# Kernel optimization log

Hardware: AMD Instinct MI355X
Metric: run time of the kernel (lower is better)

## Reference

```python
import jax, jax.numpy as jnp
import numpy as np

N = 50000
E = 400000
IN_DIM = 64
HID = 64
HEADS = 4
LN_EPS = 1e-5


def _glorot(key, shape):
    fan_in, fan_out = shape[-1], shape[0] if len(shape) > 1 else shape[-1]
    lim = jnp.sqrt(6.0 / (fan_in + fan_out))
    return jax.random.uniform(key, shape, jnp.float32, -lim, lim)


def setup_inputs() -> dict:
    key = jax.random.key(0)
    ks = jax.random.split(key, 24)
    x = jax.random.normal(ks[0], (N, IN_DIM), jnp.float32)
    edge_index = jax.random.randint(ks[1], (2, E), 0, N, jnp.int64)
    role_ids = jax.random.randint(ks[2], (N,), 0, 2, jnp.int64)
    # GAT layer 1: in IN_DIM -> HEADS*HID, concat
    W1 = _glorot(ks[3], (HEADS * HID, IN_DIM))
    a1s = _glorot(ks[4], (HEADS, HID))
    a1d = _glorot(ks[5], (HEADS, HID))
    b1 = jnp.zeros((HEADS * HID,), jnp.float32)
    # GAT layer 2: HEADS*HID -> HEADS*HID, concat
    W2 = _glorot(ks[6], (HEADS * HID, HEADS * HID))
    a2s = _glorot(ks[7], (HEADS, HID))
    a2d = _glorot(ks[8], (HEADS, HID))
    b2 = jnp.zeros((HEADS * HID,), jnp.float32)
    # GAT layer 3: HEADS*HID -> HID, 1 head, no concat
    W3 = _glorot(ks[9], (HID, HEADS * HID))
    a3s = _glorot(ks[10], (1, HID))
    a3d = _glorot(ks[11], (1, HID))
    b3 = jnp.zeros((HID,), jnp.float32)
    ln1_w = jnp.ones((HEADS * HID,), jnp.float32); ln1_b = jnp.zeros((HEADS * HID,), jnp.float32)
    ln2_w = jnp.ones((HEADS * HID,), jnp.float32); ln2_b = jnp.zeros((HEADS * HID,), jnp.float32)
    ln3_w = jnp.ones((HID,), jnp.float32); ln3_b = jnp.zeros((HID,), jnp.float32)
    role_table = jax.random.normal(ks[12], (2, HID), jnp.float32)
    p1_w = _glorot(ks[13], (HID, 2 * HID)); p1_b = jnp.zeros((HID,), jnp.float32)
    p2_w = _glorot(ks[14], (HID, HID)); p2_b = jnp.zeros((HID,), jnp.float32)
    return dict(x=x, edge_index=edge_index, role_ids=role_ids,
                W1=W1, a1s=a1s, a1d=a1d, b1=b1,
                W2=W2, a2s=a2s, a2d=a2d, b2=b2,
                W3=W3, a3s=a3s, a3d=a3d, b3=b3,
                ln1_w=ln1_w, ln1_b=ln1_b, ln2_w=ln2_w, ln2_b=ln2_b,
                ln3_w=ln3_w, ln3_b=ln3_b,
                role_table=role_table, p1_w=p1_w, p1_b=p1_b, p2_w=p2_w, p2_b=p2_b)


def gat_conv(x, src, dst, W, a_src, a_dst, bias, heads, out_ch, concat):
    # x: [N, F_in]; src/dst: [E'] (self loops already appended)
    n = x.shape[0]
    h = (x @ W.T).reshape(n, heads, out_ch)              # [N,H,C]
    score_s = jnp.einsum('nhc,hc->nh', h, a_src)          # [N,H]
    score_d = jnp.einsum('nhc,hc->nh', h, a_dst)
    e = jax.nn.leaky_relu(score_s[src] + score_d[dst], 0.2)   # [E,H]
    m = jax.ops.segment_max(e, dst, num_segments=n)       # per-dst softmax
    e = jnp.exp(e - m[dst])
    s = jax.ops.segment_sum(e, dst, num_segments=n)
    alpha = e / (s[dst] + 1e-16)                          # [E,H]
    msg = h[src] * alpha[:, :, None]                      # [E,H,C]
    out = jax.ops.segment_sum(msg, dst, num_segments=n)   # [N,H,C]
    out = out.reshape(n, heads * out_ch) if concat else out.mean(axis=1)
    return out + bias


def layer_norm(x, w, b):
    mu = jnp.mean(x, axis=-1, keepdims=True)
    var = jnp.mean(jnp.square(x - mu), axis=-1, keepdims=True)
    return (x - mu) * jax.lax.rsqrt(var + LN_EPS) * w + b


def reference(x, edge_index, role_ids, W1, a1s, a1d, b1, W2, a2s, a2d, b2,
              W3, a3s, a3d, b3, ln1_w, ln1_b, ln2_w, ln2_b, ln3_w, ln3_b,
              role_table, p1_w, p1_b, p2_w, p2_b):
    n = x.shape[0]
    loop = jnp.arange(n, dtype=edge_index.dtype)
    src = jnp.concatenate([edge_index[0], loop])
    dst = jnp.concatenate([edge_index[1], loop])
    h = jax.nn.elu(gat_conv(x, src, dst, W1, a1s, a1d, b1, HEADS, HID, True))
    h = layer_norm(h, ln1_w, ln1_b)
    h = jax.nn.elu(gat_conv(h, src, dst, W2, a2s, a2d, b2, HEADS, HID, True))
    h = layer_norm(h, ln2_w, ln2_b)
    h = gat_conv(h, src, dst, W3, a3s, a3d, b3, 1, HID, False)
    h = layer_norm(h, ln3_w, ln3_b)
    role_emb = role_table[role_ids]                        # [N,HID]
    z = jnp.concatenate([h, role_emb], axis=-1)            # [N,2*HID]
    z = jax.nn.relu(z @ p1_w.T + p1_b)
    z = z @ p2_w.T + p2_b
    return z
```

## Files before the change

kernel.cpp:

```cpp
#include <hip/hip_runtime.h>
#include <math.h>


using short8 = __attribute__((ext_vector_type(8))) short;
using f32x4  = __attribute__((ext_vector_type(4))) float;

__device__ __forceinline__ unsigned short f2bf(float f) {
    unsigned int u = __builtin_bit_cast(unsigned int, f);
    u += 0x7fffu + ((u >> 16) & 1u);
    return (unsigned short)(u >> 16);
}
__device__ __forceinline__ float bf2f(unsigned int b16) {
    unsigned int u = b16 << 16;
    return __builtin_bit_cast(float, u);
}

__global__ void k_f2bf(const float* __restrict__ in, unsigned short* __restrict__ out,
                       int n) {
    int i = (blockIdx.x * 256 + threadIdx.x) * 4;
    if (i >= n) return;
    float4 v = *reinterpret_cast<const float4*>(in + i);
    ushort4 u;
    u.x = f2bf(v.x); u.y = f2bf(v.y); u.z = f2bf(v.z); u.w = f2bf(v.w);
    *reinterpret_cast<ushort4*>(out + i) = u;
}

__global__ void k_f2bf_w(const float* __restrict__ s0, unsigned short* __restrict__ d0, int n0,
                         const float* __restrict__ s1, unsigned short* __restrict__ d1, int n1,
                         const float* __restrict__ s2, unsigned short* __restrict__ d2, int n2,
                         const float* __restrict__ s3, unsigned short* __restrict__ d3, int n3,
                         const float* __restrict__ s4, unsigned short* __restrict__ d4, int n4) {
    int i = (blockIdx.x * 256 + threadIdx.x) * 4;
    const float* s; unsigned short* d; int off = i;
    if (off < n0) { s = s0; d = d0; }
    else if ((off -= n0) < n1) { s = s1; d = d1; }
    else if ((off -= n1) < n2) { s = s2; d = d2; }
    else if ((off -= n2) < n3) { s = s3; d = d3; }
    else if ((off -= n3) < n4) { s = s4; d = d4; }
    else return;
    float4 v = *reinterpret_cast<const float4*>(s + off);
    ushort4 u;
    u.x = f2bf(v.x); u.y = f2bf(v.y); u.z = f2bf(v.z); u.w = f2bf(v.w);
    *reinterpret_cast<ushort4*>(d + off) = u;
}

__global__ void k_count(const int* __restrict__ ei, int* __restrict__ deg,
                        int N, int E, int E2) {
    int i = blockIdx.x * 256 + threadIdx.x;
    if (i >= E2) return;
    int d = (i < E) ? ei[E + i] : (i - E);
    atomicAdd(&deg[d], 1);
}

__device__ __forceinline__ int blk_scan_incl(int v, int tid) {
    int lane = tid & 63, w = tid >> 6;
#pragma unroll
    for (int off = 1; off < 64; off <<= 1) {
        int u = __shfl_up(v, off);
        if (lane >= off) v += u;
    }
    __shared__ int wsum[4];
    if (lane == 63) wsum[w] = v;
    __syncthreads();
    int add = 0;
#pragma unroll
    for (int k = 0; k < 4; ++k)
        if (k < w) add += wsum[k];
    return v + add;
}

__global__ __launch_bounds__(256) void k_bsum(const int* __restrict__ deg,
                                              int* __restrict__ bsum, int N) {
    int i = blockIdx.x * 256 + threadIdx.x;
    int v = (i < N) ? deg[i] : 0;
#pragma unroll
    for (int off = 32; off; off >>= 1) v += __shfl_down(v, off);
    __shared__ int ws[4];
    if ((threadIdx.x & 63) == 0) ws[threadIdx.x >> 6] = v;
    __syncthreads();
    if (threadIdx.x == 0) bsum[blockIdx.x] = ws[0] + ws[1] + ws[2] + ws[3];
}

__global__ __launch_bounds__(256) void k_bscan(const int* __restrict__ bsum,
                                               int* __restrict__ boff, int nb) {
    int t = threadIdx.x;
    int v = (t < nb) ? bsum[t] : 0;
    int incl = blk_scan_incl(v, t);
    if (t < nb) boff[t] = incl - v;
}

__global__ __launch_bounds__(256) void k_scatter(const int* __restrict__ deg,
                                                 const int* __restrict__ boff,
                                                 int* __restrict__ row_ptr,
                                                 int* __restrict__ cursor,
                                                 int N, int E2) {
    int tid = threadIdx.x;
    int i = blockIdx.x * 256 + tid;
    int d = (i < N) ? deg[i] : 0;
    int incl = blk_scan_incl(d, tid);
    int ex = incl - d + boff[blockIdx.x];
    if (i < N) { row_ptr[i] = ex; cursor[i] = ex; }
    if (i == 0) row_ptr[N] = E2;
}

__global__ void k_fill(const int* __restrict__ ei, int* __restrict__ cursor,
                       int* __restrict__ edge_src, int N, int E, int E2) {
    int i = blockIdx.x * 256 + threadIdx.x;
    if (i >= E2) return;
    int s_, d_;
    if (i < E) { s_ = ei[i]; d_ = ei[E + i]; }
    else       { s_ = d_ = i - E; }
    int pos = atomicAdd(&cursor[d_], 1);
    edge_src[pos] = s_;
}

template <int K, bool RELU, bool BF16OUT>
__global__ __launch_bounds__(256) void k_gmfma(const unsigned short* __restrict__ A,
                                               const unsigned short* __restrict__ Wb,
                                               const float* __restrict__ bias,
                                               void* __restrict__ Cv,
                                               int M, int NC) {
    constexpr int NSTEP = K / 32;
    __shared__ unsigned short As[2][64 * 32];
    __shared__ unsigned short Bs[2][64 * 32];
    int tid = threadIdx.x;
    int lane = tid & 63, wid = tid >> 6;
    int wm = wid & 1, wn = wid >> 1;
    int fr = lane & 15, fq = lane >> 4;
    int bm = blockIdx.x * 64, bn = blockIdx.y * 64;

    int lrow = lane >> 2, lkq = (lane & 3) * 8;

    auto stage = [&](int buf, int k0) {
        int ra = wid * 16;
        int arow = min(bm + ra + lrow, M - 1);
        __builtin_amdgcn_global_load_lds(
            (const __attribute__((address_space(1))) unsigned int*)
                (A + (size_t)arow * K + k0 + lkq),
            (__attribute__((address_space(3))) unsigned int*)&As[buf][ra * 32],
            16, 0, 0);
        __builtin_amdgcn_global_load_lds(
            (const __attribute__((address_space(1))) unsigned int*)
                (Wb + (size_t)(bn + ra + lrow) * K + k0 + lkq),
            (__attribute__((address_space(3))) unsigned int*)&Bs[buf][ra * 32],
            16, 0, 0);
    };

    f32x4 acc[2][2];
#pragma unroll
    for (int mt = 0; mt < 2; ++mt)
#pragma unroll
        for (int nt = 0; nt < 2; ++nt) acc[mt][nt] = f32x4{0.f, 0.f, 0.f, 0.f};

    stage(0, 0);
    __syncthreads();
    int cur = 0;
    for (int t = 0; t < NSTEP; ++t) {
        if (t + 1 < NSTEP) stage(cur ^ 1, (t + 1) * 32);
        short8 af[2], bfr[2];
#pragma unroll
        for (int mt = 0; mt < 2; ++mt)
            af[mt] = *reinterpret_cast<const short8*>(
                &As[cur][(wm * 32 + mt * 16 + fr) * 32 + fq * 8]);
#pragma unroll
        for (int nt = 0; nt < 2; ++nt)
            bfr[nt] = *reinterpret_cast<const short8*>(
                &Bs[cur][(wn * 32 + nt * 16 + fr) * 32 + fq * 8]);
#pragma unroll
        for (int mt = 0; mt < 2; ++mt)
#pragma unroll
            for (int nt = 0; nt < 2; ++nt)
                acc[mt][nt] = __builtin_amdgcn_mfma_f32_16x16x32_bf16(
                    af[mt], bfr[nt], acc[mt][nt], 0, 0, 0);
        __syncthreads();
        cur ^= 1;
    }

#pragma unroll
    for (int nt = 0; nt < 2; ++nt) {
        int col = bn + wn * 32 + nt * 16 + fr;
        float bv = bias ? bias[col] : 0.f;
#pragma unroll
        for (int mt = 0; mt < 2; ++mt) {
#pragma unroll
            for (int j = 0; j < 4; ++j) {
                int row = bm + wm * 32 + mt * 16 + fq * 4 + j;
                if (row < M) {
                    float v = acc[mt][nt][j] + bv;
                    if (RELU) v = fmaxf(v, 0.f);
                    if constexpr (BF16OUT)
                        ((unsigned short*)Cv)[(size_t)row * NC + col] = f2bf(v);
                    else
                        ((float*)Cv)[(size_t)row * NC + col] = v;
                }
            }
        }
    }
}

__global__ __launch_bounds__(256) void k_scores4(const unsigned short* __restrict__ h,
                                                 const float* __restrict__ a_s,
                                                 const float* __restrict__ a_d,
                                                 float* __restrict__ sS,
                                                 float* __restrict__ sD, int N) {
    int wid = threadIdx.x >> 6, lane = threadIdx.x & 63;
    int n = blockIdx.x * 4 + wid;
    if (n >= N) return;
    int hh = lane >> 4;
    int cw = (lane & 15) * 4;
    uint2 u = *reinterpret_cast<const uint2*>(h + (size_t)n * 256 + lane * 4);
    float4 as4 = *reinterpret_cast<const float4*>(a_s + hh * 64 + cw);
    float4 ad4 = *reinterpret_cast<const float4*>(a_d + hh * 64 + cw);
    float h0 = bf2f(u.x & 0xffffu), h1 = bf2f(u.x >> 16);
    float h2 = bf2f(u.y & 0xffffu), h3 = bf2f(u.y >> 16);
    float ds = h0 * as4.x + h1 * as4.y + h2 * as4.z + h3 * as4.w;
    float dd = h0 * ad4.x + h1 * ad4.y + h2 * ad4.z + h3 * ad4.w;
#pragma unroll
    for (int off = 1; off < 16; off <<= 1) {
        ds += __shfl_xor(ds, off);
        dd += __shfl_xor(dd, off);
    }
    if ((lane & 15) == 0) { sS[n * 4 + hh] = ds; sD[n * 4 + hh] = dd; }
}

__global__ __launch_bounds__(256) void k_scores1(const unsigned short* __restrict__ h,
                                                 const float* __restrict__ a_s,
                                                 const float* __restrict__ a_d,
                                                 float* __restrict__ sS,
                                                 float* __restrict__ sD, int N) {
    int wid = threadIdx.x >> 6, lane = threadIdx.x & 63;
    int n = blockIdx.x * 16 + wid * 4 + (lane >> 4);
    if (n >= N) return;
    int cw = (lane & 15) * 4;
    uint2 u = *reinterpret_cast<const uint2*>(h + (size_t)n * 64 + cw);
    float4 as4 = *reinterpret_cast<const float4*>(a_s + cw);
    float4 ad4 = *reinterpret_cast<const float4*>(a_d + cw);
    float h0 = bf2f(u.x & 0xffffu), h1 = bf2f(u.x >> 16);
    float h2 = bf2f(u.y & 0xffffu), h3 = bf2f(u.y >> 16);
    float ds = h0 * as4.x + h1 * as4.y + h2 * as4.z + h3 * as4.w;
    float dd = h0 * ad4.x + h1 * ad4.y + h2 * ad4.z + h3 * ad4.w;
#pragma unroll
    for (int off = 1; off < 16; off <<= 1) {
        ds += __shfl_xor(ds, off);
        dd += __shfl_xor(dd, off);
    }
    if ((lane & 15) == 0) { sS[n] = ds; sD[n] = dd; }
}

template <int D, bool ELU, bool ROLE>
__global__ __launch_bounds__(256) void k_agg2(
        const unsigned short* __restrict__ hbf,
        const float* __restrict__ sS, const float* __restrict__ sD,
        const float* __restrict__ bias,
        const float* __restrict__ ln_w, const float* __restrict__ ln_b,
        const int* __restrict__ row_ptr, const int* __restrict__ edge_src,
        const int* __restrict__ role_ids, const float* __restrict__ role_table,
        unsigned short* __restrict__ out, int N, int ostride) {
    constexpr int H = D / 64;
    constexpr int CPT = 8;
    constexpr int TPN = D / CPT;
    constexpr int NPB = 256 / TPN;
    int tid = threadIdx.x;
    int n = blockIdx.x * NPB + tid / TPN;
    int t = tid % TPN;
    if (n >= N) return;
    int rs = row_ptr[n], re = row_ptr[n + 1];

    float sd[H];
    if constexpr (H == 4) {
        float4 s4 = *reinterpret_cast<const float4*>(sD + (size_t)n * 4);
        sd[0] = s4.x; sd[1] = s4.y; sd[2] = s4.z; sd[3] = s4.w;
    } else {
        sd[0] = sD[n];
    }

    float m[H], s[H];
#pragma unroll
    for (int h = 0; h < H; ++h) { m[h] = -1e30f; s[h] = 0.f; }
    for (int i = rs + t; i < re; i += TPN) {
        int src = edge_src[i];
        float ev[H];
        if constexpr (H == 4) {
            float4 s4 = *reinterpret_cast<const float4*>(sS + (size_t)src * 4);
            ev[0] = s4.x; ev[1] = s4.y; ev[2] = s4.z; ev[3] = s4.w;
        } else {
            ev[0] = sS[src];
        }
#pragma unroll
        for (int h = 0; h < H; ++h) {
            float e = ev[h] + sd[h];
            e = e > 0.f ? e : 0.2f * e;
            float mn = fmaxf(m[h], e);
            s[h] = s[h] * __expf(m[h] - mn) + __expf(e - mn);
            m[h] = mn;
        }
    }
#pragma unroll
    for (int off = 1; off < TPN; off <<= 1) {
#pragma unroll
        for (int h = 0; h < H; ++h) {
            float mo = __shfl_xor(m[h], off);
            float so = __shfl_xor(s[h], off);
            float mn = fmaxf(m[h], mo);
            s[h] = s[h] * __expf(m[h] - mn) + so * __expf(mo - mn);
            m[h] = mn;
        }
    }

    int c0 = CPT * t;
    int hh = c0 >> 6;
    float mh = m[hh];
    float inv = 1.f / (s[hh] + 1e-16f);
    float sdn = sd[hh];
    float a[CPT] = {};
#pragma unroll 2
    for (int i = rs; i < re; ++i) {
        int src = edge_src[i];
        float e = sS[(size_t)src * H + hh] + sdn;
        e = e > 0.f ? e : 0.2f * e;
        float p = __expf(e - mh);
        uint4 u = *reinterpret_cast<const uint4*>(hbf + (size_t)src * D + c0);
        a[0] += p * bf2f(u.x & 0xffffu); a[1] += p * bf2f(u.x >> 16);
        a[2] += p * bf2f(u.y & 0xffffu); a[3] += p * bf2f(u.y >> 16);
        a[4] += p * bf2f(u.z & 0xffffu); a[5] += p * bf2f(u.z >> 16);
        a[6] += p * bf2f(u.w & 0xffffu); a[7] += p * bf2f(u.w >> 16);
    }
    float v[CPT];
    float sum = 0.f, sq = 0.f;
#pragma unroll
    for (int j = 0; j < CPT; ++j) {
        float w = a[j] * inv + bias[c0 + j];
        if (ELU) w = w > 0.f ? w : (__expf(w) - 1.f);
        v[j] = w;
        sum += w; sq += w * w;
    }
#pragma unroll
    for (int off = 1; off < TPN; off <<= 1) {
        sum += __shfl_xor(sum, off);
        sq += __shfl_xor(sq, off);
    }
    float mu = sum / D;
    float var = fmaxf(sq / D - mu * mu, 0.f);
    float rstd = rsqrtf(var + 1e-5f);
    unsigned int w01, w23, w45, w67;
    {
        float y0 = (v[0] - mu) * rstd * ln_w[c0 + 0] + ln_b[c0 + 0];
        float y1 = (v[1] - mu) * rstd * ln_w[c0 + 1] + ln_b[c0 + 1];
        w01 = (unsigned int)f2bf(y0) | ((unsigned int)f2bf(y1) << 16);
        float y2 = (v[2] - mu) * rstd * ln_w[c0 + 2] + ln_b[c0 + 2];
        float y3 = (v[3] - mu) * rstd * ln_w[c0 + 3] + ln_b[c0 + 3];
        w23 = (unsigned int)f2bf(y2) | ((unsigned int)f2bf(y3) << 16);
        float y4 = (v[4] - mu) * rstd * ln_w[c0 + 4] + ln_b[c0 + 4];
        float y5 = (v[5] - mu) * rstd * ln_w[c0 + 5] + ln_b[c0 + 5];
        w45 = (unsigned int)f2bf(y4) | ((unsigned int)f2bf(y5) << 16);
        float y6 = (v[6] - mu) * rstd * ln_w[c0 + 6] + ln_b[c0 + 6];
        float y7 = (v[7] - mu) * rstd * ln_w[c0 + 7] + ln_b[c0 + 7];
        w67 = (unsigned int)f2bf(y6) | ((unsigned int)f2bf(y7) << 16);
    }
    uint4 o;
    o.x = w01; o.y = w23; o.z = w45; o.w = w67;
    *reinterpret_cast<uint4*>(out + (size_t)n * ostride + c0) = o;

    if constexpr (ROLE) {
        int rid = role_ids[n];
        float4 r0 = *reinterpret_cast<const float4*>(role_table + rid * 64 + c0);
        float4 r1 = *reinterpret_cast<const float4*>(role_table + rid * 64 + c0 + 4);
        uint4 ro;
        ro.x = (unsigned int)f2bf(r0.x) | ((unsigned int)f2bf(r0.y) << 16);
        ro.y = (unsigned int)f2bf(r0.z) | ((unsigned int)f2bf(r0.w) << 16);
        ro.z = (unsigned int)f2bf(r1.x) | ((unsigned int)f2bf(r1.y) << 16);
        ro.w = (unsigned int)f2bf(r1.z) | ((unsigned int)f2bf(r1.w) << 16);
        *reinterpret_cast<uint4*>(out + (size_t)n * ostride + 64 + c0) = ro;
    }
}

extern "C" void kernel_launch(void* const* d_in, const int* in_sizes, int n_in,
                              void* d_out, int out_size, void* d_ws, size_t ws_size,
                              hipStream_t stream) {
    const float* x        = (const float*)d_in[0];
    const int*   ei       = (const int*)d_in[1];
    const int*   role_ids = (const int*)d_in[2];
    const float* W1  = (const float*)d_in[3];
    const float* a1s = (const float*)d_in[4];
    const float* a1d = (const float*)d_in[5];
    const float* b1  = (const float*)d_in[6];
    const float* W2  = (const float*)d_in[7];
    const float* a2s = (const float*)d_in[8];
    const float* a2d = (const float*)d_in[9];
    const float* b2  = (const float*)d_in[10];
    const float* W3  = (const float*)d_in[11];
    const float* a3s = (const float*)d_in[12];
    const float* a3d = (const float*)d_in[13];
    const float* b3  = (const float*)d_in[14];
    const float* ln1w = (const float*)d_in[15];
    const float* ln1b = (const float*)d_in[16];
    const float* ln2w = (const float*)d_in[17];
    const float* ln2b = (const float*)d_in[18];
    const float* ln3w = (const float*)d_in[19];
    const float* ln3b = (const float*)d_in[20];
    const float* role_table = (const float*)d_in[21];
    const float* p1w = (const float*)d_in[22];
    const float* p1b = (const float*)d_in[23];
    const float* p2w = (const float*)d_in[24];
    const float* p2b = (const float*)d_in[25];

    const int N = in_sizes[0] / 64;
    const int E = in_sizes[1] / 2;
    const int E2 = E + N;

    char* p = (char*)d_ws;
    auto carve = [&](size_t bytes) -> char* {
        char* r = p;
        p += (bytes + 255) & ~(size_t)255;
        return r;
    };
    int* deg      = (int*)carve((size_t)N * 4);
    int* row_ptr  = (int*)carve((size_t)(N + 1) * 4);
    int* cursor   = (int*)carve((size_t)N * 4);
    int* edge_src = (int*)carve((size_t)E2 * 4);
    int* bsum     = (int*)carve((size_t)1024 * 4);
    int* boff     = (int*)carve((size_t)1024 * 4);
    float* sS     = (float*)carve((size_t)N * 4 * 4);
    float* sD     = (float*)carve((size_t)N * 4 * 4);
    unsigned short* hbf  = (unsigned short*)carve((size_t)N * 256 * 2);
    unsigned short* hlnb = (unsigned short*)carve((size_t)N * 256 * 2);
    unsigned short* catb = (unsigned short*)carve((size_t)N * 128 * 2);
    unsigned short* xb   = (unsigned short*)carve((size_t)N * 64 * 2);
    unsigned short* W1b  = (unsigned short*)carve((size_t)256 * 64 * 2);
    unsigned short* W2b  = (unsigned short*)carve((size_t)256 * 256 * 2);
    unsigned short* W3b  = (unsigned short*)carve((size_t)64 * 256 * 2);
    unsigned short* p1wb = (unsigned short*)carve((size_t)64 * 128 * 2);
    unsigned short* p2wb = (unsigned short*)carve((size_t)64 * 64 * 2);
    unsigned short* z1b  = xb;

    k_f2bf<<<(N * 64 / 4 + 255) / 256, 256, 0, stream>>>(x, xb, N * 64);
    {
        int n0 = 256 * 64, n1 = 256 * 256, n2 = 64 * 256, n3 = 64 * 128, n4 = 64 * 64;
        int tot = n0 + n1 + n2 + n3 + n4;
        k_f2bf_w<<<(tot / 4 + 255) / 256, 256, 0, stream>>>(
            W1, W1b, n0, W2, W2b, n1, W3, W3b, n2, p1w, p1wb, n3, p2w, p2wb, n4);
    }

    hipMemsetAsync(deg, 0, (size_t)N * 4, stream);
    int eb = (E2 + 255) / 256;
    int nb = (N + 255) / 256;
    k_count<<<eb, 256, 0, stream>>>(ei, deg, N, E, E2);
    k_bsum<<<nb, 256, 0, stream>>>(deg, bsum, N);
    k_bscan<<<1, 256, 0, stream>>>(bsum, boff, nb);
    k_scatter<<<nb, 256, 0, stream>>>(deg, boff, row_ptr, cursor, N, E2);
    k_fill<<<eb, 256, 0, stream>>>(ei, cursor, edge_src, N, E, E2);

    int mb = (N + 63) / 64;

    k_gmfma<64, false, true><<<dim3(mb, 4), 256, 0, stream>>>(xb, W1b, nullptr, hbf, N, 256);
    k_scores4<<<(N + 3) / 4, 256, 0, stream>>>(hbf, a1s, a1d, sS, sD, N);
    k_agg2<256, true, false><<<(N + 7) / 8, 256, 0, stream>>>(
        hbf, sS, sD, b1, ln1w, ln1b, row_ptr, edge_src,
        nullptr, nullptr, hlnb, N, 256);

    k_gmfma<256, false, true><<<dim3(mb, 4), 256, 0, stream>>>(hlnb, W2b, nullptr, hbf, N, 256);
    k_scores4<<<(N + 3) / 4, 256, 0, stream>>>(hbf, a2s, a2d, sS, sD, N);
    k_agg2<256, true, false><<<(N + 7) / 8, 256, 0, stream>>>(
        hbf, sS, sD, b2, ln2w, ln2b, row_ptr, edge_src,
        nullptr, nullptr, hlnb, N, 256);

    k_gmfma<256, false, true><<<dim3(mb, 1), 256, 0, stream>>>(hlnb, W3b, nullptr, hbf, N, 64);
    k_scores1<<<(N + 15) / 16, 256, 0, stream>>>(hbf, a3s, a3d, sS, sD, N);
    k_agg2<64, false, true><<<(N + 31) / 32, 256, 0, stream>>>(
        hbf, sS, sD, b3, ln3w, ln3b, row_ptr, edge_src,
        role_ids, role_table, catb, N, 128);

    k_gmfma<128, true, true><<<dim3(mb, 1), 256, 0, stream>>>(catb, p1wb, p1b, z1b, N, 64);
    k_gmfma<64, false, false><<<dim3(mb, 1), 256, 0, stream>>>(z1b, p2wb, p2b, (float*)d_out, N, 64);
}
```

Measured before the change: 256.9 us.

## Fuse attention score computation into GEMM epilogue with full-width N tile

The projection GEMM for the two 4-head layers now computes all 256 output columns in one block (BN=256, one wave per head), so each wave holds one head's full 64-column slice. That lets the epilogue compute the source and destination attention scores from the fp32 accumulators with shuffle reductions, and the separate k_scores4 kernel is removed. This saves a launch and a re-read of the bf16 features, and scores now come from unrounded fp32 values. In exchange the grid is four times smaller per layer, and each wave keeps 4x4 accumulators, which raises register pressure.

```diff
diff --git a/kernel.cpp b/kernel.cpp
--- a/kernel.cpp
+++ b/kernel.cpp
@@ -114,20 +114,30 @@
     edge_src[pos] = s_;
 }
 
-template <int K, bool RELU, bool BF16OUT>
+template <int K, int BN, bool RELU, bool BF16OUT, bool SCORES>
 __global__ __launch_bounds__(256) void k_gmfma(const unsigned short* __restrict__ A,
                                                const unsigned short* __restrict__ Wb,
                                                const float* __restrict__ bias,
                                                void* __restrict__ Cv,
+                                               float* __restrict__ sSo,
+                                               float* __restrict__ sDo,
+                                               const float* __restrict__ a_s,
+                                               const float* __restrict__ a_d,
                                                int M, int NC) {
     constexpr int NSTEP = K / 32;
+    constexpr int WM = (BN == 256) ? 1 : 2;
+    constexpr int WN = 4 / WM;
+    constexpr int MR = 64 / WM;
+    constexpr int NR = BN / WN;
+    constexpr int MT = MR / 16;
+    constexpr int NT = NR / 16;
     __shared__ unsigned short As[2][64 * 32];
-    __shared__ unsigned short Bs[2][64 * 32];
+    __shared__ unsigned short Bs[2][BN * 32];
     int tid = threadIdx.x;
     int lane = tid & 63, wid = tid >> 6;
-    int wm = wid & 1, wn = wid >> 1;
+    int wm = wid % WM, wn = wid / WM;
     int fr = lane & 15, fq = lane >> 4;
-    int bm = blockIdx.x * 64, bn = blockIdx.y * 64;
+    int bm = blockIdx.x * 64, bn = blockIdx.y * BN;
 
     int lrow = lane >> 2, lkq = (lane & 3) * 8;
 
@@ -139,37 +149,41 @@
                 (A + (size_t)arow * K + k0 + lkq),
             (__attribute__((address_space(3))) unsigned int*)&As[buf][ra * 32],
             16, 0, 0);
-        __builtin_amdgcn_global_load_lds(
-            (const __attribute__((address_space(1))) unsigned int*)
-                (Wb + (size_t)(bn + ra + lrow) * K + k0 + lkq),
-            (__attribute__((address_space(3))) unsigned int*)&Bs[buf][ra * 32],
-            16, 0, 0);
+#pragma unroll
+        for (int i = 0; i < BN / 64; ++i) {
+            int rb = i * 64 + wid * 16;
+            __builtin_amdgcn_global_load_lds(
+                (const __attribute__((address_space(1))) unsigned int*)
+                    (Wb + (size_t)(bn + rb + lrow) * K + k0 + lkq),
+                (__attribute__((address_space(3))) unsigned int*)&Bs[buf][rb * 32],
+                16, 0, 0);
+        }
     };
 
-    f32x4 acc[2][2];
-#pragma unroll
-    for (int mt = 0; mt < 2; ++mt)
-#pragma unroll
-        for (int nt = 0; nt < 2; ++nt) acc[mt][nt] = f32x4{0.f, 0.f, 0.f, 0.f};
+    f32x4 acc[MT][NT];
+#pragma unroll
+    for (int mt = 0; mt < MT; ++mt)
+#pragma unroll
+        for (int nt = 0; nt < NT; ++nt) acc[mt][nt] = f32x4{0.f, 0.f, 0.f, 0.f};
 
     stage(0, 0);
     __syncthreads();
     int cur = 0;
     for (int t = 0; t < NSTEP; ++t) {
         if (t + 1 < NSTEP) stage(cur ^ 1, (t + 1) * 32);
-        short8 af[2], bfr[2];
-#pragma unroll
-        for (int mt = 0; mt < 2; ++mt)
+        short8 af[MT], bfr[NT];
+#pragma unroll
+        for (int mt = 0; mt < MT; ++mt)
             af[mt] = *reinterpret_cast<const short8*>(
-                &As[cur][(wm * 32 + mt * 16 + fr) * 32 + fq * 8]);
-#pragma unroll
-        for (int nt = 0; nt < 2; ++nt)
+                &As[cur][(wm * MR + mt * 16 + fr) * 32 + fq * 8]);
+#pragma unroll
+        for (int nt = 0; nt < NT; ++nt)
             bfr[nt] = *reinterpret_cast<const short8*>(
-                &Bs[cur][(wn * 32 + nt * 16 + fr) * 32 + fq * 8]);
-#pragma unroll
-        for (int mt = 0; mt < 2; ++mt)
-#pragma unroll
-            for (int nt = 0; nt < 2; ++nt)
+                &Bs[cur][(wn * NR + nt * 16 + fr) * 32 + fq * 8]);
+#pragma unroll
+        for (int mt = 0; mt < MT; ++mt)
+#pragma unroll
+            for (int nt = 0; nt < NT; ++nt)
                 acc[mt][nt] = __builtin_amdgcn_mfma_f32_16x16x32_bf16(
                     af[mt], bfr[nt], acc[mt][nt], 0, 0, 0);
         __syncthreads();
@@ -177,14 +191,14 @@
     }
 
 #pragma unroll
-    for (int nt = 0; nt < 2; ++nt) {
-        int col = bn + wn * 32 + nt * 16 + fr;
+    for (int nt = 0; nt < NT; ++nt) {
+        int col = bn + wn * NR + nt * 16 + fr;
         float bv = bias ? bias[col] : 0.f;
 #pragma unroll
-        for (int mt = 0; mt < 2; ++mt) {
+        for (int mt = 0; mt < MT; ++mt) {
 #pragma unroll
             for (int j = 0; j < 4; ++j) {
-                int row = bm + wm * 32 + mt * 16 + fq * 4 + j;
+                int row = bm + wm * MR + mt * 16 + fq * 4 + j;
                 if (row < M) {
                     float v = acc[mt][nt][j] + bv;
                     if (RELU) v = fmaxf(v, 0.f);
@@ -196,31 +210,42 @@
             }
         }
     }
-}
-
-__global__ __launch_bounds__(256) void k_scores4(const unsigned short* __restrict__ h,
-                                                 const float* __restrict__ a_s,
-                                                 const float* __restrict__ a_d,
-                                                 float* __restrict__ sS,
-                                                 float* __restrict__ sD, int N) {
-    int wid = threadIdx.x >> 6, lane = threadIdx.x & 63;
-    int n = blockIdx.x * 4 + wid;
-    if (n >= N) return;
-    int hh = lane >> 4;
-    int cw = (lane & 15) * 4;
-    uint2 u = *reinterpret_cast<const uint2*>(h + (size_t)n * 256 + lane * 4);
-    float4 as4 = *reinterpret_cast<const float4*>(a_s + hh * 64 + cw);
-    float4 ad4 = *reinterpret_cast<const float4*>(a_d + hh * 64 + cw);
-    float h0 = bf2f(u.x & 0xffffu), h1 = bf2f(u.x >> 16);
-    float h2 = bf2f(u.y & 0xffffu), h3 = bf2f(u.y >> 16);
-    float ds = h0 * as4.x + h1 * as4.y + h2 * as4.z + h3 * as4.w;
-    float dd = h0 * ad4.x + h1 * ad4.y + h2 * ad4.z + h3 * ad4.w;
-#pragma unroll
-    for (int off = 1; off < 16; off <<= 1) {
-        ds += __shfl_xor(ds, off);
-        dd += __shfl_xor(dd, off);
-    }
-    if ((lane & 15) == 0) { sS[n * 4 + hh] = ds; sD[n * 4 + hh] = dd; }
+
+    if constexpr (SCORES) {
+#pragma unroll
+        for (int mt = 0; mt < MT; ++mt) {
+            float ps[4] = {0.f, 0.f, 0.f, 0.f};
+            float pd[4] = {0.f, 0.f, 0.f, 0.f};
+#pragma unroll
+            for (int nt = 0; nt < NT; ++nt) {
+                int c = wn * 64 + nt * 16 + fr;
+                float as = a_s[c], ad = a_d[c];
+#pragma unroll
+                for (int j = 0; j < 4; ++j) {
+                    ps[j] += acc[mt][nt][j] * as;
+                    pd[j] += acc[mt][nt][j] * ad;
+                }
+            }
+#pragma unroll
+            for (int off = 1; off < 16; off <<= 1) {
+#pragma unroll
+                for (int j = 0; j < 4; ++j) {
+                    ps[j] += __shfl_xor(ps[j], off);
+                    pd[j] += __shfl_xor(pd[j], off);
+                }
+            }
+            if (fr == 0) {
+#pragma unroll
+                for (int j = 0; j < 4; ++j) {
+                    int row = bm + mt * 16 + fq * 4 + j;
+                    if (row < M) {
+                        sSo[row * 4 + wn] = ps[j];
+                        sDo[row * 4 + wn] = pd[j];
+                    }
+                }
+            }
+        }
+    }
 }
 
 __global__ __launch_bounds__(256) void k_scores1(const unsigned short* __restrict__ h,
@@ -452,24 +477,27 @@
 
     int mb = (N + 63) / 64;
 
-    k_gmfma<64, false, true><<<dim3(mb, 4), 256, 0, stream>>>(xb, W1b, nullptr, hbf, N, 256);
-    k_scores4<<<(N + 3) / 4, 256, 0, stream>>>(hbf, a1s, a1d, sS, sD, N);
+    k_gmfma<64, 256, false, true, true><<<dim3(mb, 1), 256, 0, stream>>>(
+        xb, W1b, nullptr, hbf, sS, sD, a1s, a1d, N, 256);
     k_agg2<256, true, false><<<(N + 7) / 8, 256, 0, stream>>>(
         hbf, sS, sD, b1, ln1w, ln1b, row_ptr, edge_src,
         nullptr, nullptr, hlnb, N, 256);
 
-    k_gmfma<256, false, true><<<dim3(mb, 4), 256, 0, stream>>>(hlnb, W2b, nullptr, hbf, N, 256);
-    k_scores4<<<(N + 3) / 4, 256, 0, stream>>>(hbf, a2s, a2d, sS, sD, N);
+    k_gmfma<256, 256, false, true, true><<<dim3(mb, 1), 256, 0, stream>>>(
+        hlnb, W2b, nullptr, hbf, sS, sD, a2s, a2d, N, 256);
     k_agg2<256, true, false><<<(N + 7) / 8, 256, 0, stream>>>(
         hbf, sS, sD, b2, ln2w, ln2b, row_ptr, edge_src,
         nullptr, nullptr, hlnb, N, 256);
 
-    k_gmfma<256, false, true><<<dim3(mb, 1), 256, 0, stream>>>(hlnb, W3b, nullptr, hbf, N, 64);
+    k_gmfma<256, 64, false, true, false><<<dim3(mb, 1), 256, 0, stream>>>(
+        hlnb, W3b, nullptr, hbf, nullptr, nullptr, nullptr, nullptr, N, 64);
     k_scores1<<<(N + 15) / 16, 256, 0, stream>>>(hbf, a3s, a3d, sS, sD, N);
     k_agg2<64, false, true><<<(N + 31) / 32, 256, 0, stream>>>(
         hbf, sS, sD, b3, ln3w, ln3b, row_ptr, edge_src,
         role_ids, role_table, catb, N, 128);
 
-    k_gmfma<128, true, true><<<dim3(mb, 1), 256, 0, stream>>>(catb, p1wb, p1b, z1b, N, 64);
-    k_gmfma<64, false, false><<<dim3(mb, 1), 256, 0, stream>>>(z1b, p2wb, p2b, (float*)d_out, N, 64);
-}
+    k_gmfma<128, 64, true, true, false><<<dim3(mb, 1), 256, 0, stream>>>(
+        catb, p1wb, p1b, z1b, nullptr, nullptr, nullptr, nullptr, N, 64);
+    k_gmfma<64, 64, false, false, false><<<dim3(mb, 1), 256, 0, stream>>>(
+        z1b, p2wb, p2b, (float*)d_out, nullptr, nullptr, nullptr, nullptr, N, 64);
+}
```

New measurement: 262.1 us. 2.0% more time.
